# Kernel optimization log

Measured on AMD Instinct MI355X. Metric: run time of the kernel, lower is better.

Reference implementation:

```python
import jax, jax.numpy as jnp
import numpy as np

N = 100000  # nodes
E = 1600000  # edges


def gcn_conv(x, W, b, src, dst, n_nodes):
    """PyG-style GCNConv: add self-loops, symmetric norm, linear, scatter-add, bias."""
    h = x @ W  # [N, F_out]
    loop = jnp.arange(n_nodes, dtype=src.dtype)
    s = jnp.concatenate([src, loop])  # source nodes (messages flow src -> dst)
    d = jnp.concatenate([dst, loop])
    deg = jax.ops.segment_sum(jnp.ones_like(d, dtype=h.dtype), d, num_segments=n_nodes)
    dinv = jnp.where(deg > 0, jax.lax.rsqrt(deg), 0.0)
    norm = dinv[s] * dinv[d]  # [E+N]
    msgs = h[s] * norm[:, None]  # [E+N, F_out] -- dominant memory traffic
    out = jax.ops.segment_sum(msgs, d, num_segments=n_nodes)
    return out + b


def setup_inputs() -> dict:
    key = jax.random.key(0)
    k1, k2, k3, k4 = jax.random.split(key, 4)
    x = jax.random.normal(k1, (N, 128), dtype=jnp.float32)
    edge_index = jax.random.randint(k2, (2, E), 0, N, dtype=jnp.int32)
    W1 = jax.random.normal(k3, (128, 64), dtype=jnp.float32) * (1.0 / np.sqrt(128))
    b1 = jnp.zeros((64,), dtype=jnp.float32)
    W2 = jax.random.normal(k4, (64, 16), dtype=jnp.float32) * (1.0 / np.sqrt(64))
    b2 = jnp.zeros((16,), dtype=jnp.float32)
    return {"x": x, "edge_index": edge_index, "W1": W1, "b1": b1, "W2": W2, "b2": b2}


def reference(x, edge_index, W1, b1, W2, b2):
    src, dst = edge_index[0], edge_index[1]
    h = gcn_conv(x, W1, b1, src, dst, N)
    h = jax.nn.leaky_relu(h, negative_slope=0.2)
    # dropout is identity in eval mode
    h = gcn_conv(h, W2, b2, src, dst, N)
    return jax.nn.log_softmax(h, axis=-1)
```

## Files before the change

### kernel.cpp

```cpp
#include <hip/hip_runtime.h>
#include <math.h>


#define BSHIFT 9
#define BMASK 511
#define CAP 9216
#define CAPP (CAP + 40)

typedef __bf16 bf16x8 __attribute__((ext_vector_type(8)));
typedef float f32x4 __attribute__((ext_vector_type(4)));

__device__ __forceinline__ unsigned f2b(float f) {
  unsigned u = __float_as_uint(f);
  return (u + 0x7FFF + ((u >> 16) & 1)) >> 16;
}

struct f2 { float x, y; };
__device__ __forceinline__ void addu(f2& a, unsigned u) {
  a.x += __uint_as_float(u << 16);
  a.y += __uint_as_float(u);
}
__device__ __forceinline__ void addu4(f2* a, uint4 g) {
  addu(a[0], g.x); addu(a[1], g.y); addu(a[2], g.z); addu(a[3], g.w);
}

__global__ __launch_bounds__(256) void scatterA_kernel(const int* __restrict__ src,
                                                       const int* __restrict__ dst,
                                                       int E, int chunk, int nbc,
                                                       int* __restrict__ gbcursor,
                                                       int* __restrict__ tmp) {
  __shared__ int hist[256];
  __shared__ int segcur[256];
  int tid = threadIdx.x;
  int estart = blockIdx.x * chunk;
  int eend = min(E, estart + chunk);
  hist[tid] = 0;
  __syncthreads();
  for (int i = estart + tid; i < eend; i += 256)
    atomicAdd(&hist[dst[i] >> BSHIFT], 1);
  __syncthreads();
  if (tid < nbc) {
    int c = hist[tid];
    segcur[tid] = c ? (tid * CAP + atomicAdd(&gbcursor[tid], c)) : 0;
  }
  __syncthreads();
  for (int i = estart + tid; i < eend; i += 256) {
    int d = dst[i];
    int b = d >> BSHIFT;
    int pos = atomicAdd(&segcur[b], 1);
    if (pos < (b + 1) * CAP)
      tmp[pos] = (src[i] << BSHIFT) | (d & BMASK);
  }
}

__global__ __launch_bounds__(512) void degcnt_kernel(const int* __restrict__ tmp,
                                                     const int* __restrict__ gbcursor,
                                                     int* __restrict__ degs,
                                                     float* __restrict__ dinv,
                                                     unsigned* __restrict__ h1s,
                                                     unsigned* __restrict__ t, int n) {
  __shared__ int nh[512];
  int b = blockIdx.x, tid = threadIdx.x;
  nh[tid] = 0;
  if (b == 0) {
    if (tid < 32) h1s[(size_t)n * 32 + tid] = 0u;
    else if (tid < 40) t[(size_t)n * 8 + (tid - 32)] = 0u;
  }
  __syncthreads();
  int base = b * CAP;
  int count = min(gbcursor[b], CAP);
  for (int i = tid; i < count; i += 512) atomicAdd(&nh[tmp[base + i] & BMASK], 1);
  __syncthreads();
  int v = (b << BSHIFT) + tid;
  if (v < n) {
    degs[v] = nh[tid];
    dinv[v] = rsqrtf((float)(nh[tid] + 1));
  }
}

__global__ __launch_bounds__(1024, 2) void gemm1_kernel(const float* __restrict__ x,
                                                        const float* __restrict__ W1,
                                                        const float* __restrict__ dinv,
                                                        unsigned* __restrict__ h1s, int n) {
  __shared__ unsigned wt[64 * 68];
  int tid = threadIdx.x;
  int vb = blockIdx.x * 256;

  unsigned short* wt16 = (unsigned short*)wt;
  const float4* wg = (const float4*)W1;
#pragma unroll
  for (int it = 0; it < 2; ++it) {
    int idx = it * 1024 + tid;
    int k = idx >> 4, n0 = (idx & 15) * 4;
    float4 wv = wg[idx];
    wt16[(n0 + 0) * 136 + k] = (unsigned short)f2b(wv.x);
    wt16[(n0 + 1) * 136 + k] = (unsigned short)f2b(wv.y);
    wt16[(n0 + 2) * 136 + k] = (unsigned short)f2b(wv.z);
    wt16[(n0 + 3) * 136 + k] = (unsigned short)f2b(wv.w);
  }
  __syncthreads();

  int lane = tid & 63, wid = tid >> 6;
  int m16 = lane & 15, quad = lane >> 4;
  int row_a = vb + wid * 16 + m16;
  int ra = (row_a < n) ? row_a : n - 1;
  const float4* xg = (const float4*)x + (size_t)ra * 32 + quad * 2;
  unsigned a32[4][4];
#pragma unroll
  for (int ks = 0; ks < 4; ++ks) {
    float4 v0 = xg[ks * 8];
    float4 v1 = xg[ks * 8 + 1];
    a32[ks][0] = (f2b(v0.y) << 16) | f2b(v0.x);
    a32[ks][1] = (f2b(v0.w) << 16) | f2b(v0.z);
    a32[ks][2] = (f2b(v1.y) << 16) | f2b(v1.x);
    a32[ks][3] = (f2b(v1.w) << 16) | f2b(v1.z);
  }
  const unsigned* wp = wt + m16 * 68 + quad * 4;
  f32x4 acc[4] = {};
#pragma unroll
  for (int ks = 0; ks < 4; ++ks) {
    bf16x8 a = *(const bf16x8*)a32[ks];
#pragma unroll
    for (int nt = 0; nt < 4; ++nt) {
      bf16x8 b = *(const bf16x8*)(wp + nt * 16 * 68 + ks * 16);
      acc[nt] = __builtin_amdgcn_mfma_f32_16x16x32_bf16(a, b, acc[nt], 0, 0, 0);
    }
  }
  int rbase = vb + wid * 16 + quad * 4;
  float dvv[4];
#pragma unroll
  for (int reg = 0; reg < 4; ++reg) {
    int row = rbase + reg;
    dvv[reg] = (row < n) ? dinv[row] : 0.f;
  }
  unsigned short* h16 = (unsigned short*)h1s;
#pragma unroll
  for (int nt = 0; nt < 4; ++nt) {
    int col = nt * 16 + m16;
#pragma unroll
    for (int reg = 0; reg < 4; ++reg) {
      int row = rbase + reg;
      if (row < n)
        h16[(size_t)row * 64 + col] = (unsigned short)f2b(dvv[reg] * acc[nt][reg]);
    }
  }
}

template <int NQ>
__device__ __forceinline__ void gatherTier1(const uint4* __restrict__ h1s4,
                                            const int* lcsr, int rs, int e1,
                                            int e, int c, int n, f2* a0) {
  int cv0[NQ], cv1[NQ];
#pragma unroll
  for (int q = 0; q < NQ; ++q) {
    cv0[q] = lcsr[rs + q * 8 + e];
    cv1[q] = lcsr[rs + q * 8 + 4 + e];
  }
  uint4 g[2 * NQ];
#pragma unroll
  for (int q = 0; q < NQ; ++q) {
    int k0 = rs + q * 8 + e, k1 = k0 + 4;
    int s0 = (k0 < e1) ? cv0[q] : n;
    int s1 = (k1 < e1) ? cv1[q] : n;
    g[2 * q] = h1s4[(size_t)s0 * 8 + c];
    g[2 * q + 1] = h1s4[(size_t)s1 * 8 + c];
  }
#pragma unroll
  for (int k = 0; k < 2 * NQ; ++k) addu4(a0, g[k]);
}

__global__ __launch_bounds__(1024) void agg1_fused_kernel(
    const int* __restrict__ tmp, const int* __restrict__ gbcursor,
    const uint4* __restrict__ h1s4, const float* __restrict__ dinv,
    const float* __restrict__ b1, const float* __restrict__ W2,
    const int* __restrict__ degs, int* __restrict__ row_start,
    int* __restrict__ csr, unsigned* __restrict__ t, int n) {
  __shared__ int lcsr[CAPP];
  __shared__ int nh[512];
  __shared__ int rs_s[512];
  __shared__ int lcur[512];
  __shared__ float W2s[64 * 17];
  __shared__ float b1s[64];
  __shared__ float a_s[16][2][64];
  int b = blockIdx.x, tid = threadIdx.x;
  int base = b * CAP;
  int count = min(gbcursor[b], CAP);

  if (tid < 512) {
    int v = (b << BSHIFT) + tid;
    int d = (v < n) ? degs[v] : 0;
    nh[tid] = d;
    rs_s[tid] = d;
  }
  W2s[(tid >> 4) * 17 + (tid & 15)] = W2[tid];
  if (tid < 64) b1s[tid] = b1[tid];
  __syncthreads();
  for (int off = 1; off < 512; off <<= 1) {
    int a = 0;
    if (tid < 512) { a = rs_s[tid]; if (tid >= off) a += rs_s[tid - off]; }
    __syncthreads();
    if (tid < 512) rs_s[tid] = a;
    __syncthreads();
  }
  if (tid < 512) {
    int e0 = rs_s[tid] - nh[tid];
    lcur[tid] = e0;
    rs_s[tid] = e0;
    int v = (b << BSHIFT) + tid;
    if (v < n) row_start[v] = base + e0;
  }
  __syncthreads();
  for (int i = tid; i < count; i += 1024) {
    int val = tmp[base + i];
    int pos = atomicAdd(&lcur[val & BMASK], 1);
    lcsr[pos] = val >> BSHIFT;
  }
  __syncthreads();
  for (int i = tid; i < count; i += 1024) csr[base + i] = lcsr[i];

  int wave = tid >> 6, lane = tid & 63;
  int half = lane >> 5, sub = lane & 31;
  int e = sub >> 3, c = sub & 7;
  int j = sub & 15, grp = (sub >> 4) & 1;

#pragma unroll 1
  for (int it = 0; it < 16; ++it) {
    int nl = wave * 32 + it * 2 + half;
    int v = (b << BSHIFT) + nl;
    bool valid = (v < n);
    int rs = rs_s[nl];
    int deg = nh[nl];
    int e1 = rs + deg;
    float dv = valid ? dinv[valid ? v : 0] : 0.f;

    f2 a0[4];
#pragma unroll
    for (int k = 0; k < 4; ++k) a0[k] = {0.f, 0.f};
    {
      int s = (valid && sub < 8) ? v : n;
      addu4(a0, h1s4[(size_t)s * 8 + c]);
    }
    int dm = max(deg, __shfl_xor(deg, 32, 64));
    int start;
    if (dm <= 16) {
      gatherTier1<2>(h1s4, lcsr, rs, e1, e, c, n, a0);
      start = 16;
    } else if (dm <= 24) {
      gatherTier1<3>(h1s4, lcsr, rs, e1, e, c, n, a0);
      start = 24;
    } else {
      gatherTier1<4>(h1s4, lcsr, rs, e1, e, c, n, a0);
      start = 32;
    }
    int i = rs + start;
    while (__any(i < e1)) {
      int i0 = i + e, i1 = i + 4 + e;
      int s0v = lcsr[i0];
      int s1v = lcsr[i1];
      int s0 = (i0 < e1) ? s0v : n;
      int s1 = (i1 < e1) ? s1v : n;
      addu4(a0, h1s4[(size_t)s0 * 8 + c]);
      addu4(a0, h1s4[(size_t)s1 * 8 + c]);
      i += 8;
    }
#pragma unroll
    for (int m = 8; m <= 16; m <<= 1) {
#pragma unroll
      for (int k = 0; k < 4; ++k) {
        a0[k].x += __shfl_xor(a0[k].x, m, 64);
        a0[k].y += __shfl_xor(a0[k].y, m, 64);
      }
    }
    if (sub < 8) {
#pragma unroll
      for (int k = 0; k < 4; ++k) {
        float z0 = fmaf(dv, a0[k].x, b1s[8 * sub + 2 * k]);
        float z1 = fmaf(dv, a0[k].y, b1s[8 * sub + 2 * k + 1]);
        a_s[wave][half][8 * sub + 2 * k] = fmaxf(z0, 0.2f * z0);
        a_s[wave][half][8 * sub + 2 * k + 1] = fmaxf(z1, 0.2f * z1);
      }
    }
    float p = 0.f;
#pragma unroll
    for (int q = 0; q < 16; ++q) {
      int f = grp * 16 + q;
      p = fmaf(a_s[wave][half][f], W2s[f * 17 + j], p);
    }
#pragma unroll
    for (int q = 0; q < 16; ++q) {
      int f = 32 + grp * 16 + q;
      p = fmaf(a_s[wave][half][f], W2s[f * 17 + j], p);
    }
    p += __shfl_xor(p, 16, 64);
    float pv = dv * p;
    float po = __shfl_xor(pv, 1, 64);
    if (valid && sub < 16 && !(sub & 1))
      t[(size_t)v * 8 + (sub >> 1)] = (f2b(po) << 16) | f2b(pv);
  }
}

__global__ __launch_bounds__(256) void agg2_kernel(const uint4* __restrict__ t4,
                                                   const float* __restrict__ dinv,
                                                   const int* __restrict__ row_start,
                                                   const int* __restrict__ degs,
                                                   const int* __restrict__ csr,
                                                   const float* __restrict__ b2,
                                                   float* __restrict__ out, int n) {
  int idx = blockIdx.x * 256 + threadIdx.x;
  int v = idx >> 4;
  if (v >= n) return;
  int sub = threadIdx.x & 15;
  int e = sub >> 1, c = sub & 1;
  float dv = dinv[v];
  int rs = row_start[v], e1 = rs + degs[v];
  f2 A0[4];
#pragma unroll
  for (int k = 0; k < 4; ++k) A0[k] = {0.f, 0.f};
  {
    int s = (e == 0) ? v : n;
    addu4(A0, t4[(size_t)s * 2 + c]);
  }
  int cv[4];
#pragma unroll
  for (int q = 0; q < 4; ++q) cv[q] = csr[rs + q * 8 + e];
  uint4 g[4];
#pragma unroll
  for (int q = 0; q < 4; ++q) {
    int k = rs + q * 8 + e;
    int s = (k < e1) ? cv[q] : n;
    g[q] = t4[(size_t)s * 2 + c];
  }
#pragma unroll
  for (int k = 0; k < 4; ++k) addu4(A0, g[k]);
  int i = rs + 32;
  while (i < e1) {
    int i0 = i + e;
    int sv = csr[i0];
    int s = (i0 < e1) ? sv : n;
    addu4(A0, t4[(size_t)s * 2 + c]);
    i += 8;
  }
#pragma unroll
  for (int m = 2; m <= 8; m <<= 1) {
#pragma unroll
    for (int k = 0; k < 4; ++k) {
      A0[k].x += __shfl_xor(A0[k].x, m, 64);
      A0[k].y += __shfl_xor(A0[k].y, m, 64);
    }
  }
  float4 bb0 = ((const float4*)b2)[c * 2];
  float4 bb1 = ((const float4*)b2)[c * 2 + 1];
  float z[8];
  z[0] = fmaf(dv, A0[0].x, bb0.x); z[1] = fmaf(dv, A0[0].y, bb0.y);
  z[2] = fmaf(dv, A0[1].x, bb0.z); z[3] = fmaf(dv, A0[1].y, bb0.w);
  z[4] = fmaf(dv, A0[2].x, bb1.x); z[5] = fmaf(dv, A0[2].y, bb1.y);
  z[6] = fmaf(dv, A0[3].x, bb1.z); z[7] = fmaf(dv, A0[3].y, bb1.w);
  float mx = z[0];
#pragma unroll
  for (int q = 1; q < 8; ++q) mx = fmaxf(mx, z[q]);
  mx = fmaxf(mx, __shfl_xor(mx, 1, 64));
  float ss = 0.f;
#pragma unroll
  for (int q = 0; q < 8; ++q) ss += expf(z[q] - mx);
  ss += __shfl_xor(ss, 1, 64);
  float lg = mx + logf(ss);
  if (e == 0) {
    float4 r0 = make_float4(z[0] - lg, z[1] - lg, z[2] - lg, z[3] - lg);
    float4 r1 = make_float4(z[4] - lg, z[5] - lg, z[6] - lg, z[7] - lg);
    float4* o = (float4*)out + (size_t)v * 4 + c * 2;
    o[0] = r0;
    o[1] = r1;
  }
}

extern "C" void kernel_launch(void* const* d_in, const int* in_sizes, int n_in,
                              void* d_out, int out_size, void* d_ws, size_t ws_size,
                              hipStream_t stream) {
  const float* x = (const float*)d_in[0];
  const int* edge_index = (const int*)d_in[1];
  const float* W1 = (const float*)d_in[2];
  const float* b1 = (const float*)d_in[3];
  const float* W2 = (const float*)d_in[4];
  const float* b2 = (const float*)d_in[5];
  float* out = (float*)d_out;

  int N_ = in_sizes[0] / 128;
  int E_ = in_sizes[1] / 2;
  const int* src = edge_index;
  const int* dst = edge_index + E_;
  int NBc = (N_ + BMASK) >> BSHIFT;
  int NSC = 512;
  int CHK = (E_ + NSC - 1) / NSC;

  char* ws = (char*)d_ws;
  size_t off = 0;
  auto take = [&](size_t bytes) {
    void* p = ws + off;
    off += (bytes + 255) & ~(size_t)255;
    return p;
  };
  unsigned* h1s = (unsigned*)take(((size_t)N_ + 1) * 32 * 4);
  unsigned* t = (unsigned*)take(((size_t)N_ + 1) * 8 * 4);
  int* tmp = (int*)take((size_t)NBc * CAP * 4);
  int* csr = (int*)take(((size_t)NBc * CAP + 64) * 4);
  float* dinv = (float*)take((size_t)N_ * 4);
  int* degs = (int*)take((size_t)N_ * 4);
  int* row_start = (int*)take((size_t)N_ * 4);
  int* gbcursor = (int*)take((size_t)NBc * 4);
  (void)ws_size;

  hipMemsetAsync(gbcursor, 0, (size_t)NBc * 4, stream);
  scatterA_kernel<<<NSC, 256, 0, stream>>>(src, dst, E_, CHK, NBc, gbcursor, tmp);
  degcnt_kernel<<<NBc, 512, 0, stream>>>(tmp, gbcursor, degs, dinv, h1s, t, N_);
  gemm1_kernel<<<(N_ + 255) / 256, 1024, 0, stream>>>(x, W1, dinv, h1s, N_);
  agg1_fused_kernel<<<NBc, 1024, 0, stream>>>(tmp, gbcursor, (const uint4*)h1s,
                                              dinv, b1, W2, degs, row_start, csr,
                                              t, N_);
  agg2_kernel<<<(N_ * 16 + 255) / 256, 256, 0, stream>>>((const uint4*)t, dinv,
                                                         row_start, degs, csr,
                                                         b2, out, N_);
}
```

Baseline: 196.4 us.

## Fuse degree counting into first GEMM kernel and retune scatter chunking

```diff
diff --git a/kernel.cpp b/kernel.cpp
--- a/kernel.cpp
+++ b/kernel.cpp
@@ -2,6 +2,7 @@
 #include <math.h>
 
 
+#define CHUNK 4096
 #define BSHIFT 9
 #define BMASK 511
 #define CAP 9216
@@ -26,14 +27,14 @@
 
 __global__ __launch_bounds__(256) void scatterA_kernel(const int* __restrict__ src,
                                                        const int* __restrict__ dst,
-                                                       int E, int chunk, int nbc,
+                                                       int E, int nbc,
                                                        int* __restrict__ gbcursor,
                                                        int* __restrict__ tmp) {
   __shared__ int hist[256];
   __shared__ int segcur[256];
   int tid = threadIdx.x;
-  int estart = blockIdx.x * chunk;
-  int eend = min(E, estart + chunk);
+  int estart = blockIdx.x * CHUNK;
+  int eend = min(E, estart + CHUNK);
   hist[tid] = 0;
   __syncthreads();
   for (int i = estart + tid; i < eend; i += 256)
@@ -53,38 +54,39 @@
   }
 }
 
-__global__ __launch_bounds__(512) void degcnt_kernel(const int* __restrict__ tmp,
-                                                     const int* __restrict__ gbcursor,
-                                                     int* __restrict__ degs,
-                                                     float* __restrict__ dinv,
-                                                     unsigned* __restrict__ h1s,
-                                                     unsigned* __restrict__ t, int n) {
+__global__ __launch_bounds__(1024, 1) void prep_kernel(
+    const int* __restrict__ tmp, const int* __restrict__ gbcursor,
+    const float* __restrict__ x, const float* __restrict__ W1,
+    int* __restrict__ degs, float* __restrict__ dinv,
+    unsigned* __restrict__ h1s, unsigned* __restrict__ t, int n) {
+  __shared__ unsigned wt[64 * 68];
   __shared__ int nh[512];
+  __shared__ float dl[512];
   int b = blockIdx.x, tid = threadIdx.x;
-  nh[tid] = 0;
   if (b == 0) {
     if (tid < 32) h1s[(size_t)n * 32 + tid] = 0u;
     else if (tid < 40) t[(size_t)n * 8 + (tid - 32)] = 0u;
   }
-  __syncthreads();
+  if (tid < 512) nh[tid] = 0;
+  __syncthreads();
+
+  int lane = tid & 63, wid = tid >> 6;
+  int m16 = lane & 15, quad = lane >> 4;
+
+  int rloc0 = wid * 16 + m16;
+  int row0 = (b << BSHIFT) + rloc0;
+  int r0 = (row0 < n) ? row0 : n - 1;
+  const float4* xg0 = (const float4*)x + (size_t)r0 * 32 + quad * 2;
+  float4 xv[8];
+#pragma unroll
+  for (int ks = 0; ks < 4; ++ks) {
+    xv[2 * ks] = xg0[ks * 8];
+    xv[2 * ks + 1] = xg0[ks * 8 + 1];
+  }
+
   int base = b * CAP;
   int count = min(gbcursor[b], CAP);
-  for (int i = tid; i < count; i += 512) atomicAdd(&nh[tmp[base + i] & BMASK], 1);
-  __syncthreads();
-  int v = (b << BSHIFT) + tid;
-  if (v < n) {
-    degs[v] = nh[tid];
-    dinv[v] = rsqrtf((float)(nh[tid] + 1));
-  }
-}
-
-__global__ __launch_bounds__(1024, 2) void gemm1_kernel(const float* __restrict__ x,
-                                                        const float* __restrict__ W1,
-                                                        const float* __restrict__ dinv,
-                                                        unsigned* __restrict__ h1s, int n) {
-  __shared__ unsigned wt[64 * 68];
-  int tid = threadIdx.x;
-  int vb = blockIdx.x * 256;
+  for (int i = tid; i < count; i += 1024) atomicAdd(&nh[tmp[base + i] & BMASK], 1);
 
   unsigned short* wt16 = (unsigned short*)wt;
   const float4* wg = (const float4*)W1;
@@ -100,48 +102,63 @@
   }
   __syncthreads();
 
-  int lane = tid & 63, wid = tid >> 6;
-  int m16 = lane & 15, quad = lane >> 4;
-  int row_a = vb + wid * 16 + m16;
-  int ra = (row_a < n) ? row_a : n - 1;
-  const float4* xg = (const float4*)x + (size_t)ra * 32 + quad * 2;
-  unsigned a32[4][4];
-#pragma unroll
-  for (int ks = 0; ks < 4; ++ks) {
-    float4 v0 = xg[ks * 8];
-    float4 v1 = xg[ks * 8 + 1];
-    a32[ks][0] = (f2b(v0.y) << 16) | f2b(v0.x);
-    a32[ks][1] = (f2b(v0.w) << 16) | f2b(v0.z);
-    a32[ks][2] = (f2b(v1.y) << 16) | f2b(v1.x);
-    a32[ks][3] = (f2b(v1.w) << 16) | f2b(v1.z);
-  }
+  if (tid < 512) {
+    int v = (b << BSHIFT) + tid;
+    float dvv = rsqrtf((float)(nh[tid] + 1));
+    dl[tid] = dvv;
+    if (v < n) { degs[v] = nh[tid]; dinv[v] = dvv; }
+  }
+  __syncthreads();
+
   const unsigned* wp = wt + m16 * 68 + quad * 4;
-  f32x4 acc[4] = {};
-#pragma unroll
-  for (int ks = 0; ks < 4; ++ks) {
-    bf16x8 a = *(const bf16x8*)a32[ks];
+  unsigned short* h16 = (unsigned short*)h1s;
+
+#pragma unroll 1
+  for (int pass = 0; pass < 2; ++pass) {
+    if (pass == 1) {
+      int rloc1 = 256 + wid * 16 + m16;
+      int row1 = (b << BSHIFT) + rloc1;
+      int r1 = (row1 < n) ? row1 : n - 1;
+      const float4* xg1 = (const float4*)x + (size_t)r1 * 32 + quad * 2;
+#pragma unroll
+      for (int ks = 0; ks < 4; ++ks) {
+        xv[2 * ks] = xg1[ks * 8];
+        xv[2 * ks + 1] = xg1[ks * 8 + 1];
+      }
+    }
+    unsigned a32[4][4];
+#pragma unroll
+    for (int ks = 0; ks < 4; ++ks) {
+      float4 v0 = xv[2 * ks], v1 = xv[2 * ks + 1];
+      a32[ks][0] = (f2b(v0.y) << 16) | f2b(v0.x);
+      a32[ks][1] = (f2b(v0.w) << 16) | f2b(v0.z);
+      a32[ks][2] = (f2b(v1.y) << 16) | f2b(v1.x);
+      a32[ks][3] = (f2b(v1.w) << 16) | f2b(v1.z);
+    }
+    f32x4 acc[4] = {};
+#pragma unroll
+    for (int ks = 0; ks < 4; ++ks) {
+      bf16x8 a = *(const bf16x8*)a32[ks];
+#pragma unroll
+      for (int nt = 0; nt < 4; ++nt) {
+        bf16x8 bb = *(const bf16x8*)(wp + nt * 16 * 68 + ks * 16);
+        acc[nt] = __builtin_amdgcn_mfma_f32_16x16x32_bf16(a, bb, acc[nt], 0, 0, 0);
+      }
+    }
+    int rbloc = pass * 256 + wid * 16 + quad * 4;
+    int rbase = (b << BSHIFT) + rbloc;
+    float dvv[4];
+#pragma unroll
+    for (int reg = 0; reg < 4; ++reg) dvv[reg] = dl[rbloc + reg];
 #pragma unroll
     for (int nt = 0; nt < 4; ++nt) {
-      bf16x8 b = *(const bf16x8*)(wp + nt * 16 * 68 + ks * 16);
-      acc[nt] = __builtin_amdgcn_mfma_f32_16x16x32_bf16(a, b, acc[nt], 0, 0, 0);
-    }
-  }
-  int rbase = vb + wid * 16 + quad * 4;
-  float dvv[4];
-#pragma unroll
-  for (int reg = 0; reg < 4; ++reg) {
-    int row = rbase + reg;
-    dvv[reg] = (row < n) ? dinv[row] : 0.f;
-  }
-  unsigned short* h16 = (unsigned short*)h1s;
-#pragma unroll
-  for (int nt = 0; nt < 4; ++nt) {
-    int col = nt * 16 + m16;
-#pragma unroll
-    for (int reg = 0; reg < 4; ++reg) {
-      int row = rbase + reg;
-      if (row < n)
-        h16[(size_t)row * 64 + col] = (unsigned short)f2b(dvv[reg] * acc[nt][reg]);
+      int col = nt * 16 + m16;
+#pragma unroll
+      for (int reg = 0; reg < 4; ++reg) {
+        int row = rbase + reg;
+        if (row < n)
+          h16[(size_t)row * 64 + col] = (unsigned short)f2b(dvv[reg] * acc[nt][reg]);
+      }
     }
   }
 }
@@ -389,8 +406,6 @@
   const int* src = edge_index;
   const int* dst = edge_index + E_;
   int NBc = (N_ + BMASK) >> BSHIFT;
-  int NSC = 512;
-  int CHK = (E_ + NSC - 1) / NSC;
 
   char* ws = (char*)d_ws;
   size_t off = 0;
@@ -410,9 +425,10 @@
   (void)ws_size;
 
   hipMemsetAsync(gbcursor, 0, (size_t)NBc * 4, stream);
-  scatterA_kernel<<<NSC, 256, 0, stream>>>(src, dst, E_, CHK, NBc, gbcursor, tmp);
-  degcnt_kernel<<<NBc, 512, 0, stream>>>(tmp, gbcursor, degs, dinv, h1s, t, N_);
-  gemm1_kernel<<<(N_ + 255) / 256, 1024, 0, stream>>>(x, W1, dinv, h1s, N_);
+  scatterA_kernel<<<(E_ + CHUNK - 1) / CHUNK, 256, 0, stream>>>(src, dst, E_, NBc,
+                                                                gbcursor, tmp);
+  prep_kernel<<<NBc, 1024, 0, stream>>>(tmp, gbcursor, x, W1, degs, dinv, h1s, t,
+                                        N_);
   agg1_fused_kernel<<<NBc, 1024, 0, stream>>>(tmp, gbcursor, (const uint4*)h1s,
                                               dinv, b1, W2, degs, row_start, csr,
                                               t, N_);
```

Result: faster. 191.0 us (-2.8%).
